# Kernel optimization log

Hardware: AMD Instinct MI355X
Metric: run time of the kernel (lower is better)

## Reference

```python
import jax, jax.numpy as jnp
import numpy as np

SLN, BSZ, TAG = 512, 128, 32
NEG = -1e30  # log-semiring zero (avoid literal -inf for fp16 safety)


def setup_inputs() -> dict:
    key = jax.random.key(0)
    k1, k2, k3, k4, k5, k6 = jax.random.split(key, 6)
    emission = jax.random.normal(k1, (BSZ, SLN, TAG), dtype=jnp.float32)
    length = jax.random.randint(k2, (BSZ,), 2, SLN + 1)  # clamp_min(2) semantics
    target = jax.random.randint(k3, (BSZ, SLN), 0, TAG)
    transition = jax.random.normal(k4, (TAG, TAG), dtype=jnp.float32) * 0.1
    start_transition = jax.random.normal(k5, (TAG,), dtype=jnp.float32) * 0.1
    end_transition = jax.random.normal(k6, (TAG,), dtype=jnp.float32) * 0.1
    return {
        "emission": emission,
        "length": length,
        "target": target,
        "transition": transition,
        "start_transition": start_transition,
        "end_transition": end_transition,
    }


def _crf_nll(emission, length, target, transition, start_transition, end_transition):
    # batch_first=True -> transpose to time-major, matching _verify
    em = jnp.transpose(emission, (1, 0, 2))      # [sln, bsz, tag]
    tgt = target.T                                # [sln, bsz]
    sln, bsz, tag = em.shape
    # padding_mask[t, b] = True where t >= length[b]
    pad = jnp.arange(sln)[:, None] >= length[None, :]  # [sln, bsz]

    # ---- compute_log_scores (Log semiring: mul=add, prod=sum) ----
    s = start_transition[tgt[0]]                                  # [bsz]
    p = jnp.where(pad[:, :, None], 0.0, em)                       # unit=0 at pads
    p = jnp.take_along_axis(p, tgt[:, :, None], axis=-1)[:, :, 0]  # [sln,bsz]
    p = p.sum(axis=0)                                             # [bsz]
    t = transition[tgt[:-1], tgt[1:]]                             # [sln-1,bsz]
    t = jnp.where(pad[1:], 0.0, t).sum(axis=0)                    # [bsz]
    last_tag = jnp.take_along_axis(tgt, (length - 1)[None, :], axis=0)[0]
    e = end_transition[last_tag]                                  # [bsz]
    log_score = s + p + t + e                                     # [bsz]

    # ---- compute_log_partitions (forward algorithm, chain scan) ----
    unit = jnp.where(jnp.eye(tag, dtype=bool), 0.0, NEG)          # semiring identity
    # per-step log transition matrices: [sln-1, bsz, tag, tag]
    steps = transition[None, None, :, :] + em[1:, :, None, :]
    steps = jnp.where(pad[1:, :, None, None], unit[None, None], steps)
    alpha0 = start_transition[None, :] + em[0]                    # [bsz, tag]

    def step(alpha, m):
        # log-semiring vector-matrix product: [bsz,tag] x [bsz,tag,tag]
        return jax.nn.logsumexp(alpha[:, :, None] + m, axis=1), None

    alpha, _ = jax.lax.scan(step, alpha0, steps)
    log_partition = jax.nn.logsumexp(alpha + end_transition[None, :], axis=-1)

    # fit(): reduce_tensor(-log_prob, 'sum')
    return jnp.sum(log_partition - log_score)


def reference(emission, length, target, transition, start_transition, end_transition):
    return _crf_nll(emission, length, target, transition, start_transition, end_transition)
```

## Files before the change

### kernel.cpp

```cpp
#include <hip/hip_runtime.h>

constexpr int SLN = 512, BSZ = 128, TAG = 32;
constexpr int NCH = 16, CLEN = 32;
constexpr float INVLN2 = 1.4426950408889634f;
constexpr float LN2f = 0.6931471805599453f;

typedef float f32x16 __attribute__((ext_vector_type(16)));
typedef short bfrag  __attribute__((ext_vector_type(8)));
union B8 { int i[4]; bfrag v; };

constexpr int WS_SCALE = 256;
constexpr size_t WS_MAT = 16384;

__device__ __forceinline__ float exp2_fast(float x) { return __builtin_amdgcn_exp2f(x); }
__device__ __forceinline__ float log2_fast(float x) { return __builtin_amdgcn_logf(x); }

__device__ __forceinline__ void pl32i(int& x, int& y) {
  asm("v_permlane32_swap_b32 %0, %1" : "+v"(x), "+v"(y));
}
__device__ __forceinline__ int cvtpk(float lo, float hi) {
  int r; asm("v_cvt_pk_bf16_f32 %0, %1, %2" : "=v"(r) : "v"(lo), "v"(hi)); return r;
}
__device__ __forceinline__ void gload_lds16(const float* g, float* lds_uniform) {
  __builtin_amdgcn_global_load_lds(
      (const __attribute__((address_space(1))) unsigned int*)g,
      (__attribute__((address_space(3))) unsigned int*)lds_uniform, 16, 0, 0);
}
__device__ __forceinline__ f32x16 mfma32(bfrag a, bfrag b, f32x16 c) {
  return __builtin_amdgcn_mfma_f32_32x32x16_bf16(a, b, c, 0, 0, 0);
}

template<bool PKLO>
__device__ __forceinline__ int pk2(float a, float b) {
  return PKLO ? cvtpk(a, b) : cvtpk(b, a);
}

template<bool SEM1>
__device__ __forceinline__ void mk_b(int& o0, int& o1, int& o2, int& o3,
                                     int p0, int p1, int p2, int p3) {
  if constexpr (SEM1) { pl32i(p2, p0); pl32i(p3, p1); }
  else                { pl32i(p0, p2); pl32i(p1, p3); }
  o0 = p0; o1 = p1; o2 = p2; o3 = p3;
}

template<bool SEM1, bool PKLO>
__device__ __forceinline__ void mstep(f32x16& acc, float& base, bfrag A1, bfrag A2,
                                      float4 q0, float4 q1, float4 q2, float4 q3) {
  const int bits = __builtin_amdgcn_readfirstlane(__float_as_int(acc[0]));
  const int ex = (bits >> 23) & 255;
  const float f = __int_as_float((254 - ex) << 23);
  base += (float)(ex - 127);
  const int p0 = pk2<PKLO>(acc[0] * (q0.x * f),  acc[1] * (q0.y * f));
  const int p1 = pk2<PKLO>(acc[2] * (q0.z * f),  acc[3] * (q0.w * f));
  const int p2 = pk2<PKLO>(acc[4] * (q1.x * f),  acc[5] * (q1.y * f));
  const int p3 = pk2<PKLO>(acc[6] * (q1.z * f),  acc[7] * (q1.w * f));
  const int p4 = pk2<PKLO>(acc[8] * (q2.x * f),  acc[9] * (q2.y * f));
  const int p5 = pk2<PKLO>(acc[10] * (q2.z * f), acc[11] * (q2.w * f));
  const int p6 = pk2<PKLO>(acc[12] * (q3.x * f), acc[13] * (q3.y * f));
  const int p7 = pk2<PKLO>(acc[14] * (q3.z * f), acc[15] * (q3.w * f));
  B8 B1u, B2u;
  mk_b<SEM1>(B1u.i[0], B1u.i[1], B1u.i[2], B1u.i[3], p0, p1, p2, p3);
  mk_b<SEM1>(B2u.i[0], B2u.i[1], B2u.i[2], B2u.i[3], p4, p5, p6, p7);
  f32x16 z;
#pragma unroll
  for (int r = 0; r < 16; ++r) z[r] = 0.0f;
  f32x16 t = mfma32(A1, B1u.v, z);
  acc = mfma32(A2, B2u.v, t);
}

template<bool SEM1, bool PKLO>
__device__ __forceinline__ void chunk_loop(f32x16& acc, float& base, bfrag A1, bfrag A2,
                                           const float* em_s, int count, int h) {
  if (count <= 0) return;
  const float* eb = em_s + 4 * h;
  auto LDQ = [&](int tt, float4& a, float4& b, float4& c, float4& d) {
    const float* p = eb + tt * TAG;
    a = *(const float4*)(p);
    b = *(const float4*)(p + 8);
    c = *(const float4*)(p + 16);
    d = *(const float4*)(p + 24);
  };
  int tt = count - 1;
  float4 a0, a1, a2, a3, b0, b1, b2, b3;
  LDQ(tt, a0, a1, a2, a3);
  LDQ(tt >= 1 ? tt - 1 : 0, b0, b1, b2, b3);
  while (tt >= 2) {
    mstep<SEM1, PKLO>(acc, base, A1, A2, a0, a1, a2, a3);
    LDQ(tt - 2, a0, a1, a2, a3);
    __builtin_amdgcn_sched_barrier(0);
    mstep<SEM1, PKLO>(acc, base, A1, A2, b0, b1, b2, b3);
    LDQ(tt >= 3 ? tt - 3 : 0, b0, b1, b2, b3);
    __builtin_amdgcn_sched_barrier(0);
    tt -= 2;
  }
  if (tt == 1) {
    mstep<SEM1, PKLO>(acc, base, A1, A2, a0, a1, a2, a3);
    mstep<SEM1, PKLO>(acc, base, A1, A2, b0, b1, b2, b3);
  } else {
    mstep<SEM1, PKLO>(acc, base, A1, A2, a0, a1, a2, a3);
  }
}

__global__ __launch_bounds__(64) void crf_chunk(
    const float* __restrict__ emission, const int* __restrict__ length,
    const float* __restrict__ transition, float* __restrict__ ws) {
  const int blk = blockIdx.x, lane = threadIdx.x;
  const int b = blk >> 4, c = blk & 15;
  __shared__ float em_s[CLEN * TAG];
  __shared__ float tb[TAG * 36];

  const float* gem = emission + (size_t)b * SLN * TAG;
  const int base_e = (c * CLEN + 1) * TAG;
#pragma unroll
  for (int i = 0; i < 4; ++i) {
    int o = base_e + i * 256 + lane * 4;
    o = o > (SLN * TAG - 4) ? (SLN * TAG - 4) : o;
    gload_lds16(gem + o, &em_s[i * 256]);
  }

  const int m = lane & 31, h = lane >> 5;

  int pv = lane, qv = lane + 64;
  pl32i(pv, qv);
  const bool sem1 = (__builtin_amdgcn_readfirstlane(pv) == 96);
  const bool pklo = ((cvtpk(1.0f, 2.0f) & 0xffff) == 0x3f80);

  B8 A1u, A2u;
#pragma unroll
  for (int q = 0; q < 4; ++q) {
    const int k0 = 8 * h + 2 * q;
    const float e0 = exp2_fast(transition[m * TAG + k0] * INVLN2);
    const float e1 = exp2_fast(transition[m * TAG + k0 + 1] * INVLN2);
    const float e2 = exp2_fast(transition[m * TAG + 16 + k0] * INVLN2);
    const float e3 = exp2_fast(transition[m * TAG + 16 + k0 + 1] * INVLN2);
    A1u.i[q] = pklo ? cvtpk(e0, e1) : cvtpk(e1, e0);
    A2u.i[q] = pklo ? cvtpk(e2, e3) : cvtpk(e3, e2);
  }

  const int len = length[b];
  int count = len - 1 - c * CLEN;
  count = count < 0 ? 0 : (count > CLEN ? CLEN : count);

  asm volatile("s_waitcnt vmcnt(0)" ::: "memory");

  {
    float4* p = (float4*)&em_s[lane * 16];
#pragma unroll
    for (int q = 0; q < 4; ++q) {
      float4 v = p[q];
      v.x = exp2_fast(v.x * INVLN2); v.y = exp2_fast(v.y * INVLN2);
      v.z = exp2_fast(v.z * INVLN2); v.w = exp2_fast(v.w * INVLN2);
      p[q] = v;
    }
  }

  f32x16 acc;
  float base = 0.0f;
#pragma unroll
  for (int r = 0; r < 16; ++r) {
    const int ir = (r & 3) + 8 * (r >> 2) + 4 * h;
    acc[r] = (ir == m) ? 1.0f : 0.0f;
  }

  if (sem1) {
    if (pklo) chunk_loop<true, true>(acc, base, A1u.v, A2u.v, em_s, count, h);
    else      chunk_loop<true, false>(acc, base, A1u.v, A2u.v, em_s, count, h);
  } else {
    if (pklo) chunk_loop<false, true>(acc, base, A1u.v, A2u.v, em_s, count, h);
    else      chunk_loop<false, false>(acc, base, A1u.v, A2u.v, em_s, count, h);
  }

#pragma unroll
  for (int r = 0; r < 16; ++r) {
    const int ir = (r & 3) + 8 * (r >> 2) + 4 * h;
    tb[ir * 36 + m] = acc[r];
  }
  const float* rp = &tb[m * 36 + 16 * h];
  const float4 r0 = *(const float4*)(rp);
  const float4 r1 = *(const float4*)(rp + 4);
  const float4 r2 = *(const float4*)(rp + 8);
  const float4 r3 = *(const float4*)(rp + 12);
  const int d0 = pklo ? cvtpk(r0.x, r0.y) : cvtpk(r0.y, r0.x);
  const int d1 = pklo ? cvtpk(r0.z, r0.w) : cvtpk(r0.w, r0.z);
  const int d2 = pklo ? cvtpk(r1.x, r1.y) : cvtpk(r1.y, r1.x);
  const int d3 = pklo ? cvtpk(r1.z, r1.w) : cvtpk(r1.w, r1.z);
  const int d4 = pklo ? cvtpk(r2.x, r2.y) : cvtpk(r2.y, r2.x);
  const int d5 = pklo ? cvtpk(r2.z, r2.w) : cvtpk(r2.w, r2.z);
  const int d6 = pklo ? cvtpk(r3.x, r3.y) : cvtpk(r3.y, r3.x);
  const int d7 = pklo ? cvtpk(r3.z, r3.w) : cvtpk(r3.w, r3.z);
  char* dst = (char*)ws + WS_MAT + (size_t)(b * NCH + c) * 2048 + m * 64 + h * 32;
  *(int4*)dst = make_int4(d0, d1, d2, d3);
  *(int4*)(dst + 16) = make_int4(d4, d5, d6, d7);
  if (lane == 0) ws[WS_SCALE + b * NCH + c] = base;
}

template<bool SEM1, bool PKLO>
__device__ void comb_body(int b, int lane, const float* emission,
                          const float* start_tr, const float* end_tr,
                          float* ws, float* vf) {
  const int m = lane & 31, h = lane >> 5;
  B8 B1u, B2u;
#pragma unroll
  for (int q = 0; q < 4; ++q) {
    const int k0 = 8 * h + 2 * q;
    const float e0 = exp2_fast(end_tr[k0] * INVLN2);
    const float e1 = exp2_fast(end_tr[k0 + 1] * INVLN2);
    const float e2 = exp2_fast(end_tr[16 + k0] * INVLN2);
    const float e3 = exp2_fast(end_tr[16 + k0 + 1] * INVLN2);
    const int dA = pk2<PKLO>(e0, e1), dB = pk2<PKLO>(e2, e3);
    B1u.i[q] = (m == 0) ? dA : 0;
    B2u.i[q] = (m == 0) ? dB : 0;
  }
  const char* matb = (const char*)ws + WS_MAT;
  auto LDA = [&](int c, int4& x, int4& y) {
    const char* p = matb + (size_t)(b * NCH + c) * 2048 + m * 64 + 16 * h;
    x = *(const int4*)p;
    y = *(const int4*)(p + 32);
  };
  float base_t = 0.0f;
  int4 xa, ya;
  LDA(NCH - 1, xa, ya);
  f32x16 D;
  for (int c = NCH - 1; c >= 0; --c) {
    int4 xn, yn;
    if (c > 0) LDA(c - 1, xn, yn);
    const float sc = ws[WS_SCALE + b * NCH + c];
    B8 Au, Av;
    Au.i[0] = xa.x; Au.i[1] = xa.y; Au.i[2] = xa.z; Au.i[3] = xa.w;
    Av.i[0] = ya.x; Av.i[1] = ya.y; Av.i[2] = ya.z; Av.i[3] = ya.w;
    f32x16 z;
#pragma unroll
    for (int r = 0; r < 16; ++r) z[r] = 0.0f;
    f32x16 t = mfma32(Au.v, B1u.v, z);
    D = mfma32(Av.v, B2u.v, t);
    const int bits = __builtin_amdgcn_readfirstlane(__float_as_int(D[0]));
    const int ex = (bits >> 23) & 255;
    const float f = __int_as_float((254 - ex) << 23);
    base_t += (float)(ex - 127) + sc;
#pragma unroll
    for (int r = 0; r < 16; ++r) D[r] *= f;
    if (c > 0) {
      const int p0 = pk2<PKLO>(D[0], D[1]);
      const int p1 = pk2<PKLO>(D[2], D[3]);
      const int p2 = pk2<PKLO>(D[4], D[5]);
      const int p3 = pk2<PKLO>(D[6], D[7]);
      const int p4 = pk2<PKLO>(D[8], D[9]);
      const int p5 = pk2<PKLO>(D[10], D[11]);
      const int p6 = pk2<PKLO>(D[12], D[13]);
      const int p7 = pk2<PKLO>(D[14], D[15]);
      mk_b<SEM1>(B1u.i[0], B1u.i[1], B1u.i[2], B1u.i[3], p0, p1, p2, p3);
      mk_b<SEM1>(B2u.i[0], B2u.i[1], B2u.i[2], B2u.i[3], p4, p5, p6, p7);
      xa = xn; ya = yn;
    }
  }
  if (m == 0) {
#pragma unroll
    for (int r = 0; r < 16; ++r) vf[(r & 3) + 8 * (r >> 2) + 4 * h] = D[r];
  }
  const float a0 = exp2_fast((start_tr[m] + emission[(size_t)b * SLN * TAG + m]) * INVLN2);
  float vsum = (lane < 32) ? vf[m] * a0 : 0.0f;
#pragma unroll
  for (int mm = 32; mm >= 1; mm >>= 1) vsum += __shfl_xor(vsum, mm, 64);
  if (lane == 0) ws[b] = LN2f * (log2_fast(vsum) + base_t);
}

__global__ __launch_bounds__(64) void crf_comb(
    const float* __restrict__ emission, const int* __restrict__ length,
    const int* __restrict__ target, const float* __restrict__ transition,
    const float* __restrict__ start_tr, const float* __restrict__ end_tr,
    float* __restrict__ ws) {
  const int blk = blockIdx.x, lane = threadIdx.x;
  __shared__ float vf[TAG];
  if (blk < BSZ) {
    int pv = lane, qv = lane + 64;
    pl32i(pv, qv);
    const bool sem1 = (__builtin_amdgcn_readfirstlane(pv) == 96);
    const bool pklo = ((cvtpk(1.0f, 2.0f) & 0xffff) == 0x3f80);
    if (sem1) {
      if (pklo) comb_body<true, true>(blk, lane, emission, start_tr, end_tr, ws, vf);
      else      comb_body<true, false>(blk, lane, emission, start_tr, end_tr, ws, vf);
    } else {
      if (pklo) comb_body<false, true>(blk, lane, emission, start_tr, end_tr, ws, vf);
      else      comb_body<false, false>(blk, lane, emission, start_tr, end_tr, ws, vf);
    }
  } else {
    const int b = blk - BSZ;
    const int len = length[b];
    const int* tg = target + b * SLN;
    float s = 0.f;
#pragma unroll
    for (int k0 = 0; k0 < SLN; k0 += 64) {
      const int k = k0 + lane;
      if (k < len) {
        const int tk = tg[k];
        s += emission[((size_t)b * SLN + k) * TAG + tk];
        if (k >= 1) s += transition[tg[k - 1] * TAG + tk];
      }
    }
#pragma unroll
    for (int mm = 32; mm >= 1; mm >>= 1) s += __shfl_xor(s, mm, 64);
    if (lane == 0) {
      s += start_tr[tg[0]] + end_tr[tg[len - 1]];
      ws[BSZ + b] = s;
    }
  }
}

__global__ __launch_bounds__(64) void crf_reduce_kernel(const float* __restrict__ ws,
                                                        float* __restrict__ out) {
  const int lane = threadIdx.x;
  float v = (ws[lane] - ws[BSZ + lane]) + (ws[lane + 64] - ws[BSZ + lane + 64]);
#pragma unroll
  for (int m = 32; m >= 1; m >>= 1) v += __shfl_xor(v, m, 64);
  if (lane == 0) out[0] = v;
}

extern "C" void kernel_launch(void* const* d_in, const int* in_sizes, int n_in,
                              void* d_out, int out_size, void* d_ws, size_t ws_size,
                              hipStream_t stream) {
  const float* emission   = (const float*)d_in[0];
  const int*   length     = (const int*)d_in[1];
  const int*   target     = (const int*)d_in[2];
  const float* transition = (const float*)d_in[3];
  const float* start_tr   = (const float*)d_in[4];
  const float* end_tr     = (const float*)d_in[5];
  float* ws = (float*)d_ws;

  crf_chunk<<<BSZ * NCH, 64, 0, stream>>>(emission, length, transition, ws);
  crf_comb<<<2 * BSZ, 64, 0, stream>>>(emission, length, target, transition,
                                       start_tr, end_tr, ws);
  crf_reduce_kernel<<<1, 64, 0, stream>>>(ws, (float*)d_out);
}
```

Measured before the change: 91.10 us.

## Fuse chunk, combine and reduce kernels into one launch with atomic arrival counters

Merges the three kernel launches into a single kernel. The last-arriving chunk block of each batch element runs the combine step, and the c==0 block computes the gold-path score. A global done counter hands the final reduction to whichever block arrives last. This removes two kernel launch gaps and the inter-kernel drains, at the cost of a memset launch, threadfences and atomics, and serialized combine work on late blocks.

```diff
diff --git a/kernel.cpp b/kernel.cpp
--- a/kernel.cpp
+++ b/kernel.cpp
@@ -10,6 +10,7 @@
 union B8 { int i[4]; bfrag v; };
 
 constexpr int WS_SCALE = 256;
+constexpr size_t WS_CNT = 9216;
 constexpr size_t WS_MAT = 16384;
 
 __device__ __forceinline__ float exp2_fast(float x) { return __builtin_amdgcn_exp2f(x); }
@@ -101,99 +102,6 @@
   }
 }
 
-__global__ __launch_bounds__(64) void crf_chunk(
-    const float* __restrict__ emission, const int* __restrict__ length,
-    const float* __restrict__ transition, float* __restrict__ ws) {
-  const int blk = blockIdx.x, lane = threadIdx.x;
-  const int b = blk >> 4, c = blk & 15;
-  __shared__ float em_s[CLEN * TAG];
-  __shared__ float tb[TAG * 36];
-
-  const float* gem = emission + (size_t)b * SLN * TAG;
-  const int base_e = (c * CLEN + 1) * TAG;
-#pragma unroll
-  for (int i = 0; i < 4; ++i) {
-    int o = base_e + i * 256 + lane * 4;
-    o = o > (SLN * TAG - 4) ? (SLN * TAG - 4) : o;
-    gload_lds16(gem + o, &em_s[i * 256]);
-  }
-
-  const int m = lane & 31, h = lane >> 5;
-
-  int pv = lane, qv = lane + 64;
-  pl32i(pv, qv);
-  const bool sem1 = (__builtin_amdgcn_readfirstlane(pv) == 96);
-  const bool pklo = ((cvtpk(1.0f, 2.0f) & 0xffff) == 0x3f80);
-
-  B8 A1u, A2u;
-#pragma unroll
-  for (int q = 0; q < 4; ++q) {
-    const int k0 = 8 * h + 2 * q;
-    const float e0 = exp2_fast(transition[m * TAG + k0] * INVLN2);
-    const float e1 = exp2_fast(transition[m * TAG + k0 + 1] * INVLN2);
-    const float e2 = exp2_fast(transition[m * TAG + 16 + k0] * INVLN2);
-    const float e3 = exp2_fast(transition[m * TAG + 16 + k0 + 1] * INVLN2);
-    A1u.i[q] = pklo ? cvtpk(e0, e1) : cvtpk(e1, e0);
-    A2u.i[q] = pklo ? cvtpk(e2, e3) : cvtpk(e3, e2);
-  }
-
-  const int len = length[b];
-  int count = len - 1 - c * CLEN;
-  count = count < 0 ? 0 : (count > CLEN ? CLEN : count);
-
-  asm volatile("s_waitcnt vmcnt(0)" ::: "memory");
-
-  {
-    float4* p = (float4*)&em_s[lane * 16];
-#pragma unroll
-    for (int q = 0; q < 4; ++q) {
-      float4 v = p[q];
-      v.x = exp2_fast(v.x * INVLN2); v.y = exp2_fast(v.y * INVLN2);
-      v.z = exp2_fast(v.z * INVLN2); v.w = exp2_fast(v.w * INVLN2);
-      p[q] = v;
-    }
-  }
-
-  f32x16 acc;
-  float base = 0.0f;
-#pragma unroll
-  for (int r = 0; r < 16; ++r) {
-    const int ir = (r & 3) + 8 * (r >> 2) + 4 * h;
-    acc[r] = (ir == m) ? 1.0f : 0.0f;
-  }
-
-  if (sem1) {
-    if (pklo) chunk_loop<true, true>(acc, base, A1u.v, A2u.v, em_s, count, h);
-    else      chunk_loop<true, false>(acc, base, A1u.v, A2u.v, em_s, count, h);
-  } else {
-    if (pklo) chunk_loop<false, true>(acc, base, A1u.v, A2u.v, em_s, count, h);
-    else      chunk_loop<false, false>(acc, base, A1u.v, A2u.v, em_s, count, h);
-  }
-
-#pragma unroll
-  for (int r = 0; r < 16; ++r) {
-    const int ir = (r & 3) + 8 * (r >> 2) + 4 * h;
-    tb[ir * 36 + m] = acc[r];
-  }
-  const float* rp = &tb[m * 36 + 16 * h];
-  const float4 r0 = *(const float4*)(rp);
-  const float4 r1 = *(const float4*)(rp + 4);
-  const float4 r2 = *(const float4*)(rp + 8);
-  const float4 r3 = *(const float4*)(rp + 12);
-  const int d0 = pklo ? cvtpk(r0.x, r0.y) : cvtpk(r0.y, r0.x);
-  const int d1 = pklo ? cvtpk(r0.z, r0.w) : cvtpk(r0.w, r0.z);
-  const int d2 = pklo ? cvtpk(r1.x, r1.y) : cvtpk(r1.y, r1.x);
-  const int d3 = pklo ? cvtpk(r1.z, r1.w) : cvtpk(r1.w, r1.z);
-  const int d4 = pklo ? cvtpk(r2.x, r2.y) : cvtpk(r2.y, r2.x);
-  const int d5 = pklo ? cvtpk(r2.z, r2.w) : cvtpk(r2.w, r2.z);
-  const int d6 = pklo ? cvtpk(r3.x, r3.y) : cvtpk(r3.y, r3.x);
-  const int d7 = pklo ? cvtpk(r3.z, r3.w) : cvtpk(r3.w, r3.z);
-  char* dst = (char*)ws + WS_MAT + (size_t)(b * NCH + c) * 2048 + m * 64 + h * 32;
-  *(int4*)dst = make_int4(d0, d1, d2, d3);
-  *(int4*)(dst + 16) = make_int4(d4, d5, d6, d7);
-  if (lane == 0) ws[WS_SCALE + b * NCH + c] = base;
-}
-
 template<bool SEM1, bool PKLO>
 __device__ void comb_body(int b, int lane, const float* emission,
                           const float* start_tr, const float* end_tr,
@@ -264,28 +172,124 @@
   if (lane == 0) ws[b] = LN2f * (log2_fast(vsum) + base_t);
 }
 
-__global__ __launch_bounds__(64) void crf_comb(
+__global__ __launch_bounds__(64) void crf_mega(
     const float* __restrict__ emission, const int* __restrict__ length,
     const int* __restrict__ target, const float* __restrict__ transition,
     const float* __restrict__ start_tr, const float* __restrict__ end_tr,
-    float* __restrict__ ws) {
+    float* __restrict__ ws, float* __restrict__ out) {
   const int blk = blockIdx.x, lane = threadIdx.x;
-  __shared__ float vf[TAG];
-  if (blk < BSZ) {
-    int pv = lane, qv = lane + 64;
-    pl32i(pv, qv);
-    const bool sem1 = (__builtin_amdgcn_readfirstlane(pv) == 96);
-    const bool pklo = ((cvtpk(1.0f, 2.0f) & 0xffff) == 0x3f80);
+  const int b = blk >> 4, c = blk & 15;
+  __shared__ float em_s[CLEN * TAG];
+  __shared__ float tb[TAG * 36];
+
+  int* cnt = (int*)((char*)ws + WS_CNT);
+  const float* gem = emission + (size_t)b * SLN * TAG;
+  const int base_e = (c * CLEN + 1) * TAG;
+#pragma unroll
+  for (int i = 0; i < 4; ++i) {
+    int o = base_e + i * 256 + lane * 4;
+    o = o > (SLN * TAG - 4) ? (SLN * TAG - 4) : o;
+    gload_lds16(gem + o, &em_s[i * 256]);
+  }
+
+  const int m = lane & 31, h = lane >> 5;
+
+  int pv = lane, qv = lane + 64;
+  pl32i(pv, qv);
+  const bool sem1 = (__builtin_amdgcn_readfirstlane(pv) == 96);
+  const bool pklo = ((cvtpk(1.0f, 2.0f) & 0xffff) == 0x3f80);
+
+  B8 A1u, A2u;
+#pragma unroll
+  for (int q = 0; q < 4; ++q) {
+    const int k0 = 8 * h + 2 * q;
+    const float e0 = exp2_fast(transition[m * TAG + k0] * INVLN2);
+    const float e1 = exp2_fast(transition[m * TAG + k0 + 1] * INVLN2);
+    const float e2 = exp2_fast(transition[m * TAG + 16 + k0] * INVLN2);
+    const float e3 = exp2_fast(transition[m * TAG + 16 + k0 + 1] * INVLN2);
+    A1u.i[q] = pklo ? cvtpk(e0, e1) : cvtpk(e1, e0);
+    A2u.i[q] = pklo ? cvtpk(e2, e3) : cvtpk(e3, e2);
+  }
+
+  const int len = length[b];
+  int count = len - 1 - c * CLEN;
+  count = count < 0 ? 0 : (count > CLEN ? CLEN : count);
+
+  asm volatile("s_waitcnt vmcnt(0)" ::: "memory");
+
+  {
+    float4* p = (float4*)&em_s[lane * 16];
+#pragma unroll
+    for (int q = 0; q < 4; ++q) {
+      float4 v = p[q];
+      v.x = exp2_fast(v.x * INVLN2); v.y = exp2_fast(v.y * INVLN2);
+      v.z = exp2_fast(v.z * INVLN2); v.w = exp2_fast(v.w * INVLN2);
+      p[q] = v;
+    }
+  }
+
+  f32x16 acc;
+  float base = 0.0f;
+#pragma unroll
+  for (int r = 0; r < 16; ++r) {
+    const int ir = (r & 3) + 8 * (r >> 2) + 4 * h;
+    acc[r] = (ir == m) ? 1.0f : 0.0f;
+  }
+
+  if (sem1) {
+    if (pklo) chunk_loop<true, true>(acc, base, A1u.v, A2u.v, em_s, count, h);
+    else      chunk_loop<true, false>(acc, base, A1u.v, A2u.v, em_s, count, h);
+  } else {
+    if (pklo) chunk_loop<false, true>(acc, base, A1u.v, A2u.v, em_s, count, h);
+    else      chunk_loop<false, false>(acc, base, A1u.v, A2u.v, em_s, count, h);
+  }
+
+#pragma unroll
+  for (int r = 0; r < 16; ++r) {
+    const int ir = (r & 3) + 8 * (r >> 2) + 4 * h;
+    tb[ir * 36 + m] = acc[r];
+  }
+  const float* rp = &tb[m * 36 + 16 * h];
+  const float4 r0 = *(const float4*)(rp);
+  const float4 r1 = *(const float4*)(rp + 4);
+  const float4 r2 = *(const float4*)(rp + 8);
+  const float4 r3 = *(const float4*)(rp + 12);
+  const int d0 = pklo ? cvtpk(r0.x, r0.y) : cvtpk(r0.y, r0.x);
+  const int d1 = pklo ? cvtpk(r0.z, r0.w) : cvtpk(r0.w, r0.z);
+  const int d2 = pklo ? cvtpk(r1.x, r1.y) : cvtpk(r1.y, r1.x);
+  const int d3 = pklo ? cvtpk(r1.z, r1.w) : cvtpk(r1.w, r1.z);
+  const int d4 = pklo ? cvtpk(r2.x, r2.y) : cvtpk(r2.y, r2.x);
+  const int d5 = pklo ? cvtpk(r2.z, r2.w) : cvtpk(r2.w, r2.z);
+  const int d6 = pklo ? cvtpk(r3.x, r3.y) : cvtpk(r3.y, r3.x);
+  const int d7 = pklo ? cvtpk(r3.z, r3.w) : cvtpk(r3.w, r3.z);
+  char* dst = (char*)ws + WS_MAT + (size_t)(b * NCH + c) * 2048 + m * 64 + h * 32;
+  *(int4*)dst = make_int4(d0, d1, d2, d3);
+  *(int4*)(dst + 16) = make_int4(d4, d5, d6, d7);
+  if (lane == 0) ws[WS_SCALE + b * NCH + c] = base;
+
+  __threadfence();
+  int arr = 0;
+  if (lane == 0) arr = atomicAdd(&cnt[b], 1);
+  arr = __shfl(arr, 0, 64);
+
+  int done_old = -1;
+
+  if (arr == NCH - 1) {
+    __threadfence();
     if (sem1) {
-      if (pklo) comb_body<true, true>(blk, lane, emission, start_tr, end_tr, ws, vf);
-      else      comb_body<true, false>(blk, lane, emission, start_tr, end_tr, ws, vf);
+      if (pklo) comb_body<true, true>(b, lane, emission, start_tr, end_tr, ws, tb);
+      else      comb_body<true, false>(b, lane, emission, start_tr, end_tr, ws, tb);
     } else {
-      if (pklo) comb_body<false, true>(blk, lane, emission, start_tr, end_tr, ws, vf);
-      else      comb_body<false, false>(blk, lane, emission, start_tr, end_tr, ws, vf);
+      if (pklo) comb_body<false, true>(b, lane, emission, start_tr, end_tr, ws, tb);
+      else      comb_body<false, false>(b, lane, emission, start_tr, end_tr, ws, tb);
     }
-  } else {
-    const int b = blk - BSZ;
-    const int len = length[b];
+    __threadfence();
+    if (lane == 0) done_old = atomicAdd(&cnt[BSZ], 1);
+    done_old = __shfl(done_old, 0, 64);
+    if (done_old == 2 * BSZ - 1) goto reduce;
+  }
+
+  if (c == 0) {
     const int* tg = target + b * SLN;
     float s = 0.f;
 #pragma unroll
@@ -299,20 +303,22 @@
     }
 #pragma unroll
     for (int mm = 32; mm >= 1; mm >>= 1) s += __shfl_xor(s, mm, 64);
-    if (lane == 0) {
-      s += start_tr[tg[0]] + end_tr[tg[len - 1]];
-      ws[BSZ + b] = s;
-    }
-  }
-}
-
-__global__ __launch_bounds__(64) void crf_reduce_kernel(const float* __restrict__ ws,
-                                                        float* __restrict__ out) {
-  const int lane = threadIdx.x;
-  float v = (ws[lane] - ws[BSZ + lane]) + (ws[lane + 64] - ws[BSZ + lane + 64]);
-#pragma unroll
-  for (int m = 32; m >= 1; m >>= 1) v += __shfl_xor(v, m, 64);
-  if (lane == 0) out[0] = v;
+    if (lane == 0) ws[BSZ + b] = s + start_tr[tg[0]] + end_tr[tg[len - 1]];
+    __threadfence();
+    if (lane == 0) done_old = atomicAdd(&cnt[BSZ], 1);
+    done_old = __shfl(done_old, 0, 64);
+    if (done_old == 2 * BSZ - 1) goto reduce;
+  }
+  return;
+
+reduce:
+  __threadfence();
+  {
+    float v = (ws[lane] - ws[BSZ + lane]) + (ws[lane + 64] - ws[BSZ + lane + 64]);
+#pragma unroll
+    for (int mm = 32; mm >= 1; mm >>= 1) v += __shfl_xor(v, mm, 64);
+    if (lane == 0) out[0] = v;
+  }
 }
 
 extern "C" void kernel_launch(void* const* d_in, const int* in_sizes, int n_in,
@@ -326,8 +332,7 @@
   const float* end_tr     = (const float*)d_in[5];
   float* ws = (float*)d_ws;
 
-  crf_chunk<<<BSZ * NCH, 64, 0, stream>>>(emission, length, transition, ws);
-  crf_comb<<<2 * BSZ, 64, 0, stream>>>(emission, length, target, transition,
-                                       start_tr, end_tr, ws);
-  crf_reduce_kernel<<<1, 64, 0, stream>>>(ws, (float*)d_out);
-}
+  hipMemsetAsync((char*)d_ws + WS_CNT, 0, 1024, stream);
+  crf_mega<<<BSZ * NCH, 64, 0, stream>>>(emission, length, target, transition,
+                                         start_tr, end_tr, ws, (float*)d_out);
+}
```

Measured after the change: 249.5 us. 174% more time.
